# Kernel tuning notes

Measured on AMD Instinct MI355X. Metric: run time of the kernel, lower is better.

## Reference

```python
import jax, jax.numpy as jnp
import numpy as np

HIDDEN = 4096
NUM_EXPERTS = 64
TOP_K = 2


def setup_inputs() -> dict:
    key = jax.random.key(0)
    k1, k2, k3 = jax.random.split(key, 3)
    hidden_states = jax.random.normal(k1, (4, 4096, HIDDEN), dtype=jnp.float32)
    # nn.Linear(hidden_size, num_experts): weight [num_experts, hidden], bias [num_experts]
    bound = 1.0 / np.sqrt(HIDDEN)
    gate_w = jax.random.uniform(k2, (NUM_EXPERTS, HIDDEN), dtype=jnp.float32, minval=-bound, maxval=bound)
    gate_b = jax.random.uniform(k3, (NUM_EXPERTS,), dtype=jnp.float32, minval=-bound, maxval=bound)
    return {"hidden_states": hidden_states, "gate_w": gate_w, "gate_b": gate_b}


def reference(hidden_states, gate_w, gate_b):
    b, s, h = hidden_states.shape
    x = hidden_states.reshape(-1, h)                      # [N, H], N = b*s
    router_logits = jnp.einsum('nh,eh->ne', x, gate_w) + gate_b  # [N, E]
    top_logits, selected_experts = jax.lax.top_k(router_logits, TOP_K)  # [N, K]
    routing_weights = jax.nn.softmax(top_logits, axis=-1)  # [N, K]
    aux_loss = jnp.float32(0.0)
    return routing_weights, selected_experts, router_logits, aux_loss
```

## Files before the change

kernel.cpp:

```cpp
#include <hip/hip_runtime.h>
#include <math.h>
#include <stdint.h>

#define HIDDEN  4096
#define NEXP    64
#define TOKS    64
#define KCH     128
#define NCHK    (HIDDEN / KCH)
#define X_FL    (TOKS * KCH)
#define PAR_FL  16384

typedef __bf16 bf16x8 __attribute__((ext_vector_type(8)));
typedef float  f32x4  __attribute__((ext_vector_type(4)));

union BfU { uint4 u; bf16x8 b; };

static __device__ __forceinline__ void cvt_hilo(const float* x8, bf16x8& hi, bf16x8& lo) {
#pragma unroll
    for (int j = 0; j < 8; ++j) {
        const float x = x8[j];
        const __bf16 h = (__bf16)x;
        const float  r = x - (float)h;
        hi[j] = h;
        lo[j] = (__bf16)r;
    }
}

__device__ __forceinline__ void gload_lds16(const void* g, void* l) {
    __builtin_amdgcn_global_load_lds(
        (const __attribute__((address_space(1))) void*)g,
        (__attribute__((address_space(3))) void*)l, 16, 0, 0);
}

__global__ __launch_bounds__(512) void wconv_kernel(
    const float* __restrict__ W, ushort* __restrict__ wsHi, ushort* __restrict__ wsLo)
{
    const int gid = blockIdx.x * blockDim.x + threadIdx.x;
    const int S = gid >> 8;
    const int e = (gid >> 6) & 3;
    const int l = gid & 63;
    const int row = 16 * e + (l & 15);
    const int k0  = 32 * S + 8 * (l >> 4);
    const float* src = W + (size_t)row * HIDDEN + k0;
    float x8[8];
    *(float4*)&x8[0] = *(const float4*)src;
    *(float4*)&x8[4] = *(const float4*)(src + 4);
    BfU hi, lo;
    cvt_hilo(x8, hi.b, lo.b);
    const size_t o = ((size_t)(S * 4 + e) * 64 + l) * 8;
    *(uint4*)(wsHi + o) = hi.u;
    *(uint4*)(wsLo + o) = lo.u;
}

__global__ __launch_bounds__(1024, 1) void router_mfma_kernel(
    const float* __restrict__ X,
    const ushort* __restrict__ wsHi, const ushort* __restrict__ wsLo,
    const float* __restrict__ Bv, float* __restrict__ out, int nTok)
{
    __shared__ float smem[2 * PAR_FL];

    const int tid = threadIdx.x;
    const int wv  = tid >> 6;
    const int tg  = wv >> 2;
    const int kh  = wv & 3;
    const int l   = tid & 63;
    const int g   = l >> 4;
    const int cr  = l & 15;
    const int t0  = blockIdx.x * TOKS;

    const float* XgS[2];
    int xdst[2];
#pragma unroll
    for (int r = 0; r < 2; ++r) {
        const int q   = 2 * wv + r;
        const int row = 2 * q + (l >> 5);
        XgS[r]  = X + (size_t)(t0 + row) * HIDDEN + (((l & 31) ^ (row & 7)) << 2);
        xdst[r] = 2 * q * KCH;
    }
    const ushort* BhS = wsHi + (size_t)wv * 512 + (size_t)l * 8;
    const ushort* BlS = wsLo + (size_t)wv * 512 + (size_t)l * 8;
    const int bhdst = X_FL + wv * 256;
    const int bldst = X_FL + 4096 + wv * 256;

    const int m8   = cr & 7;
    const int rowX = (16 * tg + cr) * KCH;
    const int gA0  = (8 * kh + ((2 * g + 0) ^ m8)) << 2;
    const int gA1  = (8 * kh + ((2 * g + 1) ^ m8)) << 2;

    f32x4 acc[4] = {{0.f,0.f,0.f,0.f},{0.f,0.f,0.f,0.f},{0.f,0.f,0.f,0.f},{0.f,0.f,0.f,0.f}};

#pragma unroll
    for (int r = 0; r < 2; ++r) gload_lds16(XgS[r], smem + xdst[r]);
    gload_lds16(BhS, smem + bhdst);
    gload_lds16(BlS, smem + bldst);
#pragma unroll
    for (int r = 0; r < 2; ++r) gload_lds16(XgS[r] + KCH, smem + PAR_FL + xdst[r]);
    gload_lds16(BhS + 8192, smem + PAR_FL + bhdst);
    gload_lds16(BlS + 8192, smem + PAR_FL + bldst);

#pragma unroll 1
    for (int c = 0; c < NCHK; ++c) {
        if (c + 1 < NCHK) asm volatile("s_waitcnt vmcnt(4)" ::: "memory");
        else              asm volatile("s_waitcnt vmcnt(0)" ::: "memory");
        __builtin_amdgcn_s_barrier();
        const int p = c & 1;
        {
            const float*  xb = smem + p * PAR_FL;
            const ushort* bh = (const ushort*)(xb + X_FL) + (4 * kh) * 512 + l * 8;
            const ushort* bl = bh + 8192;
            float x8[8];
            *(float4*)&x8[0] = *(const float4*)(xb + rowX + gA0);
            *(float4*)&x8[4] = *(const float4*)(xb + rowX + gA1);
            bf16x8 xh, xo; cvt_hilo(x8, xh, xo);
#pragma unroll
            for (int e = 0; e < 4; ++e) {
                BfU ph, pl;
                ph.u = *(const uint4*)(bh + e * 512);
                pl.u = *(const uint4*)(bl + e * 512);
                acc[e] = __builtin_amdgcn_mfma_f32_16x16x32_bf16(xh, ph.b, acc[e], 0, 0, 0);
                acc[e] = __builtin_amdgcn_mfma_f32_16x16x32_bf16(xo, ph.b, acc[e], 0, 0, 0);
                acc[e] = __builtin_amdgcn_mfma_f32_16x16x32_bf16(xh, pl.b, acc[e], 0, 0, 0);
            }
        }
        __builtin_amdgcn_s_barrier();
        if (c + 2 < NCHK) {
            float* pb = smem + p * PAR_FL;
            const int ko = (c + 2) * KCH;
            const size_t bo = (size_t)(c + 2) * 8192;
#pragma unroll
            for (int r = 0; r < 2; ++r) gload_lds16(XgS[r] + ko, pb + xdst[r]);
            gload_lds16(BhS + bo, pb + bhdst);
            gload_lds16(BlS + bo, pb + bldst);
        }
    }

    __syncthreads();

    float (*tiles)[64][68] = (float (*)[64][68])smem;
    float* tt = smem + 4 * 64 * 68;

#pragma unroll
    for (int e = 0; e < 4; ++e)
#pragma unroll
        for (int i = 0; i < 4; ++i)
            tiles[kh][16 * tg + 4 * g + i][16 * e + cr] = acc[e][i];
    __syncthreads();

    const size_t offSel = (size_t)nTok * 2;
    const size_t offLog = (size_t)nTok * 4;

    {
        const int tok = tid >> 4;
        const int e4  = (tid & 15) * 4;
        const float4 s0 = *(const float4*)&tiles[0][tok][e4];
        const float4 s1 = *(const float4*)&tiles[1][tok][e4];
        const float4 s2 = *(const float4*)&tiles[2][tok][e4];
        const float4 s3 = *(const float4*)&tiles[3][tok][e4];
        const float4 bb = *(const float4*)(Bv + e4);
        const float4 r = make_float4(s0.x + s1.x + s2.x + s3.x + bb.x,
                                     s0.y + s1.y + s2.y + s3.y + bb.y,
                                     s0.z + s1.z + s2.z + s3.z + bb.z,
                                     s0.w + s1.w + s2.w + s3.w + bb.w);
        *(float4*)(out + offLog + (size_t)(t0 + tok) * NEXP + e4) = r;
        tt[(e4 + 0) * 65 + tok] = r.x;
        tt[(e4 + 1) * 65 + tok] = r.y;
        tt[(e4 + 2) * 65 + tok] = r.z;
        tt[(e4 + 3) * 65 + tok] = r.w;
    }
    __syncthreads();

    if (tid < 64) {
        const int t = tid;
        float m1 = -INFINITY, m2 = -INFINITY;
        int i1 = 0, i2 = 0;
#pragma unroll
        for (int e = 0; e < NEXP; ++e) {
            const float v = tt[e * 65 + t];
            if (v > m1)      { m2 = m1; i2 = i1; m1 = v; i1 = e; }
            else if (v > m2) { m2 = v; i2 = e; }
        }
        const float ex  = expf(m2 - m1);
        const float inv = 1.0f / (1.0f + ex);
        *(float2*)(out + (size_t)(t0 + t) * 2)          = make_float2(inv, ex * inv);
        *(float2*)(out + offSel + (size_t)(t0 + t) * 2) = make_float2((float)i1, (float)i2);
    }

    if (blockIdx.x == 0 && tid == 0)
        out[offLog + (size_t)nTok * NEXP] = 0.0f;
}

extern "C" void kernel_launch(void* const* d_in, const int* in_sizes, int n_in,
                              void* d_out, int out_size, void* d_ws, size_t ws_size,
                              hipStream_t stream)
{
    const float* X  = (const float*)d_in[0];
    const float* W  = (const float*)d_in[1];
    const float* Bv = (const float*)d_in[2];
    float* out = (float*)d_out;
    const int nTok = in_sizes[0] / HIDDEN;
    ushort* wsHi = (ushort*)d_ws;
    ushort* wsLo = wsHi + (size_t)NEXP * HIDDEN;

    wconv_kernel<<<256, 128, 0, stream>>>(W, wsHi, wsLo);
    router_mfma_kernel<<<nTok / TOKS, 1024, 0, stream>>>(X, wsHi, wsLo, Bv, out, nTok);
}
```

Measured before the change: 70.63 us.

## Fuse weight bf16 hi/lo split into router kernel, drop separate conversion launch

Removes the separate weight-conversion kernel. Each block now loads fp32 gate weights straight into registers, splits them into bf16 hi/lo pairs and writes them into the LDS double buffer one chunk ahead of use. The software pipeline is reworked so that register prefetch of the weights overlaps the MFMA work. This saves a kernel launch and the workspace round trip. In exchange, every block (256 of them) repeats the weight conversion and adds LDS stores, and it now waits on vmcnt(0) every iteration, which may expose load latency for X.

```diff
diff --git a/kernel.cpp b/kernel.cpp
--- a/kernel.cpp
+++ b/kernel.cpp
@@ -32,29 +32,9 @@
         (__attribute__((address_space(3))) void*)l, 16, 0, 0);
 }
 
-__global__ __launch_bounds__(512) void wconv_kernel(
-    const float* __restrict__ W, ushort* __restrict__ wsHi, ushort* __restrict__ wsLo)
-{
-    const int gid = blockIdx.x * blockDim.x + threadIdx.x;
-    const int S = gid >> 8;
-    const int e = (gid >> 6) & 3;
-    const int l = gid & 63;
-    const int row = 16 * e + (l & 15);
-    const int k0  = 32 * S + 8 * (l >> 4);
-    const float* src = W + (size_t)row * HIDDEN + k0;
-    float x8[8];
-    *(float4*)&x8[0] = *(const float4*)src;
-    *(float4*)&x8[4] = *(const float4*)(src + 4);
-    BfU hi, lo;
-    cvt_hilo(x8, hi.b, lo.b);
-    const size_t o = ((size_t)(S * 4 + e) * 64 + l) * 8;
-    *(uint4*)(wsHi + o) = hi.u;
-    *(uint4*)(wsLo + o) = lo.u;
-}
-
 __global__ __launch_bounds__(1024, 1) void router_mfma_kernel(
     const float* __restrict__ X,
-    const ushort* __restrict__ wsHi, const ushort* __restrict__ wsLo,
+    const float* __restrict__ W,
     const float* __restrict__ Bv, float* __restrict__ out, int nTok)
 {
     __shared__ float smem[2 * PAR_FL];
@@ -77,10 +57,10 @@
         XgS[r]  = X + (size_t)(t0 + row) * HIDDEN + (((l & 31) ^ (row & 7)) << 2);
         xdst[r] = 2 * q * KCH;
     }
-    const ushort* BhS = wsHi + (size_t)wv * 512 + (size_t)l * 8;
-    const ushort* BlS = wsLo + (size_t)wv * 512 + (size_t)l * 8;
-    const int bhdst = X_FL + wv * 256;
-    const int bldst = X_FL + 4096 + wv * 256;
+
+    const float* Wg  = W + (size_t)(16 * (wv & 3) + cr) * HIDDEN + 32 * (wv >> 2) + 8 * g;
+    const int bHiDst = X_FL + wv * 256 + l * 4;
+    const int bLoDst = bHiDst + 4096;
 
     const int m8   = cr & 7;
     const int rowX = (16 * tg + cr) * KCH;
@@ -88,22 +68,42 @@
     const int gA1  = (8 * kh + ((2 * g + 1) ^ m8)) << 2;
 
     f32x4 acc[4] = {{0.f,0.f,0.f,0.f},{0.f,0.f,0.f,0.f},{0.f,0.f,0.f,0.f},{0.f,0.f,0.f,0.f}};
-
+    float4 wSa0, wSa1, wSb0, wSb1;
+
+    wSa0 = *(const float4*)(Wg);
+    wSa1 = *(const float4*)(Wg + 4);
 #pragma unroll
     for (int r = 0; r < 2; ++r) gload_lds16(XgS[r], smem + xdst[r]);
-    gload_lds16(BhS, smem + bhdst);
-    gload_lds16(BlS, smem + bldst);
 #pragma unroll
     for (int r = 0; r < 2; ++r) gload_lds16(XgS[r] + KCH, smem + PAR_FL + xdst[r]);
-    gload_lds16(BhS + 8192, smem + PAR_FL + bhdst);
-    gload_lds16(BlS + 8192, smem + PAR_FL + bldst);
-
-#pragma unroll 1
-    for (int c = 0; c < NCHK; ++c) {
-        if (c + 1 < NCHK) asm volatile("s_waitcnt vmcnt(4)" ::: "memory");
-        else              asm volatile("s_waitcnt vmcnt(0)" ::: "memory");
+    asm volatile("s_waitcnt vmcnt(4)" ::: "memory");
+    {
+        float x8[8];
+        *(float4*)&x8[0] = wSa0; *(float4*)&x8[4] = wSa1;
+        BfU hi, lo; cvt_hilo(x8, hi.b, lo.b);
+        *(uint4*)&smem[bHiDst] = hi.u;
+        *(uint4*)&smem[bLoDst] = lo.u;
+    }
+    wSb0 = *(const float4*)(Wg + KCH);
+    wSb1 = *(const float4*)(Wg + KCH + 4);
+    asm volatile("s_waitcnt lgkmcnt(0)" ::: "memory");
+
+    auto iter = [&](int c, float4& s0, float4& s1, float4& d0, float4& d1) {
+        asm volatile("s_waitcnt vmcnt(0)" ::: "memory");
         __builtin_amdgcn_s_barrier();
         const int p = c & 1;
+        if (c + 1 < NCHK) {
+            float* bb = smem + ((c + 1) & 1) * PAR_FL;
+            float x8[8];
+            *(float4*)&x8[0] = s0; *(float4*)&x8[4] = s1;
+            BfU hi, lo; cvt_hilo(x8, hi.b, lo.b);
+            *(uint4*)&bb[bHiDst] = hi.u;
+            *(uint4*)&bb[bLoDst] = lo.u;
+        }
+        if (c + 2 < NCHK) {
+            d0 = *(const float4*)(Wg + (size_t)(c + 2) * KCH);
+            d1 = *(const float4*)(Wg + (size_t)(c + 2) * KCH + 4);
+        }
         {
             const float*  xb = smem + p * PAR_FL;
             const ushort* bh = (const ushort*)(xb + X_FL) + (4 * kh) * 512 + l * 8;
@@ -122,16 +122,20 @@
                 acc[e] = __builtin_amdgcn_mfma_f32_16x16x32_bf16(xh, pl.b, acc[e], 0, 0, 0);
             }
         }
+        asm volatile("s_waitcnt lgkmcnt(0)" ::: "memory");
         __builtin_amdgcn_s_barrier();
         if (c + 2 < NCHK) {
             float* pb = smem + p * PAR_FL;
             const int ko = (c + 2) * KCH;
-            const size_t bo = (size_t)(c + 2) * 8192;
 #pragma unroll
             for (int r = 0; r < 2; ++r) gload_lds16(XgS[r] + ko, pb + xdst[r]);
-            gload_lds16(BhS + bo, pb + bhdst);
-            gload_lds16(BlS + bo, pb + bldst);
-        }
+        }
+    };
+
+#pragma unroll 1
+    for (int cc = 0; cc < NCHK; cc += 2) {
+        iter(cc,     wSb0, wSb1, wSa0, wSa1);
+        iter(cc + 1, wSa0, wSa1, wSb0, wSb1);
     }
 
     __syncthreads();
@@ -198,9 +202,5 @@
     const float* Bv = (const float*)d_in[2];
     float* out = (float*)d_out;
     const int nTok = in_sizes[0] / HIDDEN;
-    ushort* wsHi = (ushort*)d_ws;
-    ushort* wsLo = wsHi + (size_t)NEXP * HIDDEN;
-
-    wconv_kernel<<<256, 128, 0, stream>>>(W, wsHi, wsLo);
-    router_mfma_kernel<<<nTok / TOKS, 1024, 0, stream>>>(X, wsHi, wsLo, Bv, out, nTok);
-}
+    router_mfma_kernel<<<nTok / TOKS, 1024, 0, stream>>>(X, W, Bv, out, nTok);
+}
```

Result: slower. 76.75 us (+8.7%).

## Split router GEMM along K into two half-kernels with separate combine pass

Applied to the files above, without the earlier changes.

Replaces the single 1024-thread router kernel with a split-K GEMM. Each 512-thread block computes a 64-token tile over half of the hidden dimension, using a smaller 64-wide K chunk and two blocks per CU. A separate combine kernel adds the two partial logit sets plus bias, then does top-2 and softmax. This doubles the grid (512 blocks vs 256) for better CU occupancy and load balance, at the cost of an extra kernel launch and a round trip of partial logits through global memory.

```diff
diff --git a/kernel.cpp b/kernel.cpp
--- a/kernel.cpp
+++ b/kernel.cpp
@@ -2,13 +2,14 @@
 #include <math.h>
 #include <stdint.h>
 
-#define HIDDEN  4096
-#define NEXP    64
-#define TOKS    64
-#define KCH     128
-#define NCHK    (HIDDEN / KCH)
-#define X_FL    (TOKS * KCH)
-#define PAR_FL  16384
+#define HIDDEN 4096
+#define NEXP   64
+#define TOKS   64
+#define KBLK   2048
+#define KCH    64
+#define NCHK   (KBLK / KCH)
+#define X_FL   (TOKS * KCH)
+#define PAR_FL (X_FL + 2 * 2048)
 
 typedef __bf16 bf16x8 __attribute__((ext_vector_type(8)));
 typedef float  f32x4  __attribute__((ext_vector_type(4)));
@@ -52,35 +53,38 @@
     *(uint4*)(wsLo + o) = lo.u;
 }
 
-__global__ __launch_bounds__(1024, 1) void router_mfma_kernel(
+__global__ __launch_bounds__(512, 2) void gemm_half_kernel(
     const float* __restrict__ X,
     const ushort* __restrict__ wsHi, const ushort* __restrict__ wsLo,
-    const float* __restrict__ Bv, float* __restrict__ out, int nTok)
+    float* __restrict__ outLog, float* __restrict__ wsP, int nTok)
 {
     __shared__ float smem[2 * PAR_FL];
 
     const int tid = threadIdx.x;
     const int wv  = tid >> 6;
-    const int tg  = wv >> 2;
-    const int kh  = wv & 3;
+    const int tg  = wv >> 1;
+    const int kh  = wv & 1;
     const int l   = tid & 63;
     const int g   = l >> 4;
     const int cr  = l & 15;
-    const int t0  = blockIdx.x * TOKS;
+    const int bx  = blockIdx.x;
+    const int h   = bx & 1;
+    const int t0  = (bx >> 1) * TOKS;
 
     const float* XgS[2];
     int xdst[2];
 #pragma unroll
     for (int r = 0; r < 2; ++r) {
-        const int q   = 2 * wv + r;
-        const int row = 2 * q + (l >> 5);
-        XgS[r]  = X + (size_t)(t0 + row) * HIDDEN + (((l & 31) ^ (row & 7)) << 2);
-        xdst[r] = 2 * q * KCH;
-    }
-    const ushort* BhS = wsHi + (size_t)wv * 512 + (size_t)l * 8;
-    const ushort* BlS = wsLo + (size_t)wv * 512 + (size_t)l * 8;
+        const int q    = 2 * wv + r;
+        const int srow = 4 * q + (l >> 4);
+        const int sgr  = (l & 8) | ((l & 7) ^ (srow & 7));
+        XgS[r]  = X + (size_t)(t0 + srow) * HIDDEN + h * KBLK + sgr * 4;
+        xdst[r] = 4 * q * KCH;
+    }
+    const ushort* BhS = wsHi + (size_t)h * 131072 + (size_t)wv * 512 + (size_t)l * 8;
+    const ushort* BlS = wsLo + (size_t)h * 131072 + (size_t)wv * 512 + (size_t)l * 8;
     const int bhdst = X_FL + wv * 256;
-    const int bldst = X_FL + 4096 + wv * 256;
+    const int bldst = X_FL + 2048 + wv * 256;
 
     const int m8   = cr & 7;
     const int rowX = (16 * tg + cr) * KCH;
@@ -95,8 +99,8 @@
     gload_lds16(BlS, smem + bldst);
 #pragma unroll
     for (int r = 0; r < 2; ++r) gload_lds16(XgS[r] + KCH, smem + PAR_FL + xdst[r]);
-    gload_lds16(BhS + 8192, smem + PAR_FL + bhdst);
-    gload_lds16(BlS + 8192, smem + PAR_FL + bldst);
+    gload_lds16(BhS + 4096, smem + PAR_FL + bhdst);
+    gload_lds16(BlS + 4096, smem + PAR_FL + bldst);
 
 #pragma unroll 1
     for (int c = 0; c < NCHK; ++c) {
@@ -107,7 +111,7 @@
         {
             const float*  xb = smem + p * PAR_FL;
             const ushort* bh = (const ushort*)(xb + X_FL) + (4 * kh) * 512 + l * 8;
-            const ushort* bl = bh + 8192;
+            const ushort* bl = bh + 4096;
             float x8[8];
             *(float4*)&x8[0] = *(const float4*)(xb + rowX + gA0);
             *(float4*)&x8[4] = *(const float4*)(xb + rowX + gA1);
@@ -126,7 +130,7 @@
         if (c + 2 < NCHK) {
             float* pb = smem + p * PAR_FL;
             const int ko = (c + 2) * KCH;
-            const size_t bo = (size_t)(c + 2) * 8192;
+            const size_t bo = (size_t)(c + 2) * 4096;
 #pragma unroll
             for (int r = 0; r < 2; ++r) gload_lds16(XgS[r] + ko, pb + xdst[r]);
             gload_lds16(BhS + bo, pb + bhdst);
@@ -137,8 +141,6 @@
     __syncthreads();
 
     float (*tiles)[64][68] = (float (*)[64][68])smem;
-    float* tt = smem + 4 * 64 * 68;
-
 #pragma unroll
     for (int e = 0; e < 4; ++e)
 #pragma unroll
@@ -146,26 +148,48 @@
             tiles[kh][16 * tg + 4 * g + i][16 * e + cr] = acc[e][i];
     __syncthreads();
 
+    {
+        float* dst = (h ? wsP : outLog) + (size_t)t0 * NEXP;
+        const int tok = tid >> 3;
+        const int e8  = (tid & 7) * 8;
+        float v[8];
+#pragma unroll
+        for (int j = 0; j < 8; ++j)
+            v[j] = tiles[0][tok][e8 + j] + tiles[1][tok][e8 + j];
+        float* rowp = dst + (size_t)tok * NEXP + e8;
+        *(float4*)rowp       = make_float4(v[0], v[1], v[2], v[3]);
+        *(float4*)(rowp + 4) = make_float4(v[4], v[5], v[6], v[7]);
+    }
+}
+
+__global__ __launch_bounds__(256) void combine_kernel(
+    const float* __restrict__ wsP,
+    const float* __restrict__ Bv,
+    float* __restrict__ out, int nTok)
+{
+    __shared__ float tt[64 * 65];
+    const int tid = threadIdx.x;
+    const int t0  = blockIdx.x * TOKS;
     const size_t offSel = (size_t)nTok * 2;
     const size_t offLog = (size_t)nTok * 4;
-
-    {
-        const int tok = tid >> 4;
-        const int e4  = (tid & 15) * 4;
-        const float4 s0 = *(const float4*)&tiles[0][tok][e4];
-        const float4 s1 = *(const float4*)&tiles[1][tok][e4];
-        const float4 s2 = *(const float4*)&tiles[2][tok][e4];
-        const float4 s3 = *(const float4*)&tiles[3][tok][e4];
+    float*       L = out + offLog + (size_t)t0 * NEXP;
+    const float* P = wsP + (size_t)t0 * NEXP;
+
+#pragma unroll
+    for (int r = 0; r < 4; ++r) {
+        const int idx = r * 256 + tid;
+        const int tok = idx >> 4;
+        const int e4  = (idx & 15) * 4;
+        const float4 a  = *(const float4*)(L + tok * NEXP + e4);
+        const float4 b  = *(const float4*)(P + tok * NEXP + e4);
         const float4 bb = *(const float4*)(Bv + e4);
-        const float4 r = make_float4(s0.x + s1.x + s2.x + s3.x + bb.x,
-                                     s0.y + s1.y + s2.y + s3.y + bb.y,
-                                     s0.z + s1.z + s2.z + s3.z + bb.z,
-                                     s0.w + s1.w + s2.w + s3.w + bb.w);
-        *(float4*)(out + offLog + (size_t)(t0 + tok) * NEXP + e4) = r;
-        tt[(e4 + 0) * 65 + tok] = r.x;
-        tt[(e4 + 1) * 65 + tok] = r.y;
-        tt[(e4 + 2) * 65 + tok] = r.z;
-        tt[(e4 + 3) * 65 + tok] = r.w;
+        const float4 s = make_float4(a.x + b.x + bb.x, a.y + b.y + bb.y,
+                                     a.z + b.z + bb.z, a.w + b.w + bb.w);
+        *(float4*)(L + tok * NEXP + e4) = s;
+        tt[(e4 + 0) * 65 + tok] = s.x;
+        tt[(e4 + 1) * 65 + tok] = s.y;
+        tt[(e4 + 2) * 65 + tok] = s.z;
+        tt[(e4 + 3) * 65 + tok] = s.w;
     }
     __syncthreads();
 
@@ -181,8 +205,8 @@
         }
         const float ex  = expf(m2 - m1);
         const float inv = 1.0f / (1.0f + ex);
-        *(float2*)(out + (size_t)(t0 + t) * 2)          = make_float2(inv, ex * inv);
-        *(float2*)(out + offSel + (size_t)(t0 + t) * 2) = make_float2((float)i1, (float)i2);
+        *(float2*)(out + (size_t)(t0 + tid) * 2)          = make_float2(inv, ex * inv);
+        *(float2*)(out + offSel + (size_t)(t0 + tid) * 2) = make_float2((float)i1, (float)i2);
     }
 
     if (blockIdx.x == 0 && tid == 0)
@@ -197,10 +221,14 @@
     const float* W  = (const float*)d_in[1];
     const float* Bv = (const float*)d_in[2];
     float* out = (float*)d_out;
-    const int nTok = in_sizes[0] / HIDDEN;
+    const int nTok  = in_sizes[0] / HIDDEN;
+    const int tiles = nTok / TOKS;
     ushort* wsHi = (ushort*)d_ws;
     ushort* wsLo = wsHi + (size_t)NEXP * HIDDEN;
+    float*  wsP  = (float*)(wsLo + (size_t)NEXP * HIDDEN);
+    float*  outLog = out + (size_t)nTok * 4;
 
     wconv_kernel<<<256, 128, 0, stream>>>(W, wsHi, wsLo);
-    router_mfma_kernel<<<nTok / TOKS, 1024, 0, stream>>>(X, wsHi, wsLo, Bv, out, nTok);
-}
+    gemm_half_kernel<<<2 * tiles, 512, 0, stream>>>(X, wsHi, wsLo, outLog, wsP, nTok);
+    combine_kernel<<<tiles, 256, 0, stream>>>(wsP, Bv, out, nTok);
+}
```

Measured after the change: 67.03 us (median of 2 runs). 1.05x faster.
